# Optimization experiments

Measured on AMD Instinct MI355X. Metric: run time of the kernel, lower is better.

The kernel has to match this reference:

```python
import jax, jax.numpy as jnp
import numpy as np

FIELD_DIMS = [50000] * 24
NUM_FIELDS = len(FIELD_DIMS)
EMBED_DIM = 16
ATTN_SIZE = 32
TOTAL_VOCAB = int(np.sum(FIELD_DIMS))
OFFSETS = jnp.asarray(np.concatenate([[0], np.cumsum(FIELD_DIMS)[:-1]]), dtype=jnp.int64)
# all unordered field pairs (i < j)
_ROWS, _COLS = np.triu_indices(NUM_FIELDS, k=1)
ROWS = jnp.asarray(_ROWS)
COLS = jnp.asarray(_COLS)


def setup_inputs() -> dict:
    key = jax.random.key(0)
    ks = jax.random.split(key, 9)
    B = 16384
    x = jax.random.randint(ks[0], (B, NUM_FIELDS), 0, 50000, dtype=jnp.int64)
    s = 0.05
    return {
        "x": x,
        "embed_table": jax.random.normal(ks[1], (TOTAL_VOCAB, EMBED_DIM), jnp.float32) * s,
        "linear_table": jax.random.normal(ks[2], (TOTAL_VOCAB, 1), jnp.float32) * s,
        "linear_bias": jnp.zeros((1,), jnp.float32),
        "attn_W": jax.random.normal(ks[3], (EMBED_DIM, ATTN_SIZE), jnp.float32) * s,
        "attn_b": jnp.zeros((ATTN_SIZE,), jnp.float32),
        "proj_w": jax.random.normal(ks[4], (ATTN_SIZE, 1), jnp.float32) * s,
        "proj_b": jnp.zeros((1,), jnp.float32),
        "fc_w": jax.random.normal(ks[5], (EMBED_DIM, 1), jnp.float32) * s,
        "fc_b": jnp.zeros((1,), jnp.float32),
    }


def reference(x, embed_table, linear_table, linear_bias, attn_W, attn_b, proj_w, proj_b, fc_w, fc_b):
    idx = x + OFFSETS[None, :]                      # [B, F] global row ids
    emb = embed_table[idx]                          # [B, F, E]
    linear_term = linear_table[idx].sum(axis=1) + linear_bias  # [B, 1]
    # pairwise elementwise products
    inner = emb[:, ROWS, :] * emb[:, COLS, :]       # [B, P, E]
    # attention MLP over pairs
    h = jax.nn.relu(jnp.einsum('bpe,ea->bpa', inner, attn_W) + attn_b)  # [B, P, A]
    scores = jnp.einsum('bpa,ao->bpo', h, proj_w) + proj_b              # [B, P, 1]
    attn = jax.nn.softmax(scores, axis=1)           # softmax over pairs
    pooled = jnp.sum(attn * inner, axis=1)          # [B, E]
    cross_term = pooled @ fc_w + fc_b               # [B, 1]
    return linear_term + cross_term
```

## Files before the change

kernel.cpp:

```cpp
#include <hip/hip_runtime.h>
#include <hip/hip_bf16.h>
#include <float.h>


#define FN 24
#define ED 16
#define AS 32
#define NP 276
#define NT 9
#define LASTV 20
#define EPITCH 20
#define RPW 2
#define NTHR 256
#define FIELD_SIZE 50000

typedef __attribute__((ext_vector_type(8)))  short bf16x8;
typedef __attribute__((ext_vector_type(16))) float f32x16;
typedef __attribute__((ext_vector_type(2)))  float f32x2;

union BFR { int i[4]; bf16x8 v; };
union F4P { float4 f4; f32x2 p[2]; };

__device__ __forceinline__ short f2bf(float x) {
    union { __hip_bfloat16 h; short s; } u;
    u.h = __float2bfloat16(x);
    return u.s;
}

__device__ __forceinline__ void gather_embed(const float* __restrict__ et,
                                             int idxv, int lane,
                                             float4& a, float4& b) {
    const int f0 = lane >> 2, q0 = lane & 3;
    const int id0 = __shfl(idxv, f0, 64);
    const int id1 = __shfl(idxv, 16 + f0, 64);
    a = ((const float4*)(et + (size_t)id0 * ED))[q0];
    if (lane < 32)
        b = ((const float4*)(et + (size_t)id1 * ED))[q0];
}

__device__ __forceinline__ void write_embed(float* __restrict__ buf, int lane,
                                            const float4& a, const float4& b) {
    const int f0 = lane >> 2, q0 = lane & 3;
    *(float4*)&buf[f0 * EPITCH + q0 * 4] = a;
    if (lane < 32)
        *(float4*)&buf[(16 + f0) * EPITCH + q0 * 4] = b;
}

__global__ __launch_bounds__(NTHR, 4) void afm_kernel(
    const int*   __restrict__ x,
    const float* __restrict__ embed_table,
    const float* __restrict__ linear_table,
    const float* __restrict__ linear_bias,
    const float* __restrict__ attn_W,
    const float* __restrict__ attn_b,
    const float* __restrict__ proj_w,
    const float* __restrict__ fc_w,
    const float* __restrict__ fc_b,
    float*       __restrict__ out,
    int B)
{
    __shared__ float emb_s[NTHR / 64][2][FN * EPITCH];
    __shared__ int   pko_s[NT * 32];

    const int tid  = threadIdx.x;
    const int wave = tid >> 6;
    const int lane = tid & 63;
    const int half = lane >> 5;
    const int col  = lane & 31;
    const int e0   = half * 8;
    const int w0   = (blockIdx.x * (NTHR / 64) + wave) * RPW;

    for (int s = tid; s < NT * 32; s += NTHR) {
        const int p = (s < NP) ? s : (NP - 1);
        const int q = (NP - 1) - p;
        int m = (int)((sqrtf((float)(8 * q + 1)) + 1.0f) * 0.5f);
        if (m * (m + 1) / 2 <= q) ++m;
        if ((m - 1) * m / 2 > q) --m;
        const int fi = (FN - 1) - m;
        const int fj = fi + 1 + (p - (NP - m * (m + 1) / 2));
        pko_s[s] = ((fi * (EPITCH * 4)) << 16) | (fj * (EPITCH * 4));
    }

    int idxr[RPW];
#pragma unroll
    for (int k = 0; k < RPW; ++k) {
        const int r = w0 + k, rc = (r < B) ? r : (B - 1);
        idxr[k] = (lane < FN) ? (x[rc * FN + lane] + lane * FIELD_SIZE) : 0;
    }

    bf16x8 aW;
#pragma unroll
    for (int i = 0; i < 8; ++i) aW[i] = f2bf(attn_W[(e0 + i) * AS + col]);
    f32x16 biasC;
    f32x2  pw2[8];
#pragma unroll
    for (int r = 0; r < 16; ++r) {
        const int a = (r & 3) + 8 * (r >> 2) + 4 * half;
        biasC[r] = attn_b[a];
    }
#pragma unroll
    for (int r2 = 0; r2 < 8; ++r2) {
        const int a0 = (2 * r2 & 3) + 8 * (2 * r2 >> 2) + 4 * half;
        pw2[r2].x = proj_w[a0];
        pw2[r2].y = proj_w[a0 + 1];
    }
    f32x2 fcw2[4];
#pragma unroll
    for (int i = 0; i < 4; ++i) {
        fcw2[i].x = fc_w[e0 + 2 * i];
        fcw2[i].y = fc_w[e0 + 2 * i + 1];
    }
    const float cbias = linear_bias[0] + fc_b[0];

    float linv = (lane < FN) ? linear_table[idxr[0]] : 0.f;
    {
        float4 ga, gb;
        gather_embed(embed_table, idxr[0], lane, ga, gb);
        write_embed(emb_s[wave][0], lane, ga, gb);
    }

    __syncthreads();
    int pk[NT];
#pragma unroll
    for (int t = 0; t < NT; ++t) pk[t] = pko_s[t * 32 + col];

#pragma unroll
    for (int k = 0; k < RPW; ++k) {
        const int row = w0 + k;
        float4 na, nb; float linn = 0.f;
        if (k + 1 < RPW) {
            linn = (lane < FN) ? linear_table[idxr[k + 1]] : 0.f;
            gather_embed(embed_table, idxr[k + 1], lane, na, nb);
        }

        const char* embb = (const char*)emb_s[wave][k & 1] + half * 32;
        float m = -FLT_MAX, ssum = 0.f, gacc = 0.f;
#pragma unroll
        for (int t = 0; t < NT; ++t) {
            const int oi = pk[t] >> 16;
            const int oj = pk[t] & 0xffff;
            F4P xi0, xi1, xj0, xj1;
            xi0.f4 = *(const float4*)(embb + oi);
            xi1.f4 = *(const float4*)(embb + oi + 16);
            xj0.f4 = *(const float4*)(embb + oj);
            xj1.f4 = *(const float4*)(embb + oj + 16);
            const f32x2 P0 = xi0.p[0] * xj0.p[0];
            const f32x2 P1 = xi0.p[1] * xj0.p[1];
            const f32x2 P2 = xi1.p[0] * xj1.p[0];
            const f32x2 P3 = xi1.p[1] * xj1.p[1];
            f32x2 G = P0 * fcw2[0];
            G = __builtin_elementwise_fma(P1, fcw2[1], G);
            G = __builtin_elementwise_fma(P2, fcw2[2], G);
            G = __builtin_elementwise_fma(P3, fcw2[3], G);
            const float gv = G.x + G.y;
            BFR u;
            u.i[0] = __builtin_amdgcn_perm(__float_as_int(P0.y), __float_as_int(P0.x), 0x07060302);
            u.i[1] = __builtin_amdgcn_perm(__float_as_int(P1.y), __float_as_int(P1.x), 0x07060302);
            u.i[2] = __builtin_amdgcn_perm(__float_as_int(P2.y), __float_as_int(P2.x), 0x07060302);
            u.i[3] = __builtin_amdgcn_perm(__float_as_int(P3.y), __float_as_int(P3.x), 0x07060302);
            const f32x16 c = __builtin_amdgcn_mfma_f32_32x32x16_bf16(aW, u.v, biasC, 0, 0, 0);
            f32x2 sac; sac.x = 0.f; sac.y = 0.f;
            f32x2 z2;  z2.x = 0.f;  z2.y = 0.f;
#pragma unroll
            for (int r2 = 0; r2 < 8; ++r2) {
                f32x2 h; h.x = c[2 * r2]; h.y = c[2 * r2 + 1];
                h = __builtin_elementwise_max(h, z2);
                sac = __builtin_elementwise_fma(h, pw2[r2], sac);
            }
            float s = sac.x + sac.y;
            s += __shfl_xor(s, 32, 64);
            const bool valid = (t < NT - 1) || (col < LASTV);
            s = valid ? s : -FLT_MAX;
            const float mn   = fmaxf(m, s);
            const float cold = __expf(m - mn);
            const float e    = __expf(s - mn);
            ssum = fmaf(ssum, cold, e);
            gacc = fmaf(gacc, cold, e * gv);
            m = mn;
        }

        float M = m;
#pragma unroll
        for (int off = 16; off; off >>= 1) M = fmaxf(M, __shfl_xor(M, off, 64));
        const float rs = __expf(m - M);
        ssum *= rs; gacc *= rs;
#pragma unroll
        for (int off = 16; off; off >>= 1) ssum += __shfl_xor(ssum, off, 64);
#pragma unroll
        for (int off = 32; off; off >>= 1) gacc += __shfl_xor(gacc, off, 64);
        float lin = linv;
#pragma unroll
        for (int off = 32; off; off >>= 1) lin += __shfl_xor(lin, off, 64);

        if (row < B && lane == 0)
            out[row] = lin + cbias + gacc / ssum;

        if (k + 1 < RPW) {
            write_embed(emb_s[wave][(k + 1) & 1], lane, na, nb);
            linv = linn;
        }
    }
}

extern "C" void kernel_launch(void* const* d_in, const int* in_sizes, int n_in,
                              void* d_out, int out_size, void* d_ws, size_t ws_size,
                              hipStream_t stream) {
    const int*   x            = (const int*)  d_in[0];
    const float* embed_table  = (const float*)d_in[1];
    const float* linear_table = (const float*)d_in[2];
    const float* linear_bias  = (const float*)d_in[3];
    const float* attn_W       = (const float*)d_in[4];
    const float* attn_b       = (const float*)d_in[5];
    const float* proj_w       = (const float*)d_in[6];
    const float* fc_w         = (const float*)d_in[8];
    const float* fc_b         = (const float*)d_in[9];
    float* out = (float*)d_out;

    const int B = in_sizes[0] / FN;
    const int rows_per_block = (NTHR / 64) * RPW;
    const int grid = (B + rows_per_block - 1) / rows_per_block;
    afm_kernel<<<grid, NTHR, 0, stream>>>(x, embed_table, linear_table,
                                          linear_bias, attn_W, attn_b, proj_w,
                                          fc_w, fc_b, out, B);
}
```

Before: 142.8 us.

## Process one row per wave and replace online softmax with two-pass softmax

Each wave now handles a single batch row instead of two, which removes the double-buffered prefetch of the next row's embeddings and doubles the grid size. Scores and fc-projected values for all pair tiles are kept in registers, and the softmax is done in two passes (global max, then exp-sum) instead of the online rescaling recurrence. The intent is fewer expf calls, a shorter dependency chain and more parallel waves to hide gather latency. The cost is losing the software pipelining of the next row's gather and repeating per-block setup (pair table, weights) for every row.

```diff
diff --git a/kernel.cpp b/kernel.cpp
--- a/kernel.cpp
+++ b/kernel.cpp
@@ -10,7 +10,6 @@
 #define NT 9
 #define LASTV 20
 #define EPITCH 20
-#define RPW 2
 #define NTHR 256
 #define FIELD_SIZE 50000
 
@@ -27,25 +26,6 @@
     return u.s;
 }
 
-__device__ __forceinline__ void gather_embed(const float* __restrict__ et,
-                                             int idxv, int lane,
-                                             float4& a, float4& b) {
-    const int f0 = lane >> 2, q0 = lane & 3;
-    const int id0 = __shfl(idxv, f0, 64);
-    const int id1 = __shfl(idxv, 16 + f0, 64);
-    a = ((const float4*)(et + (size_t)id0 * ED))[q0];
-    if (lane < 32)
-        b = ((const float4*)(et + (size_t)id1 * ED))[q0];
-}
-
-__device__ __forceinline__ void write_embed(float* __restrict__ buf, int lane,
-                                            const float4& a, const float4& b) {
-    const int f0 = lane >> 2, q0 = lane & 3;
-    *(float4*)&buf[f0 * EPITCH + q0 * 4] = a;
-    if (lane < 32)
-        *(float4*)&buf[(16 + f0) * EPITCH + q0 * 4] = b;
-}
-
 __global__ __launch_bounds__(NTHR, 4) void afm_kernel(
     const int*   __restrict__ x,
     const float* __restrict__ embed_table,
@@ -59,7 +39,7 @@
     float*       __restrict__ out,
     int B)
 {
-    __shared__ float emb_s[NTHR / 64][2][FN * EPITCH];
+    __shared__ float emb_s[NTHR / 64][FN * EPITCH];
     __shared__ int   pko_s[NT * 32];
 
     const int tid  = threadIdx.x;
@@ -68,7 +48,8 @@
     const int half = lane >> 5;
     const int col  = lane & 31;
     const int e0   = half * 8;
-    const int w0   = (blockIdx.x * (NTHR / 64) + wave) * RPW;
+    const int row  = blockIdx.x * (NTHR / 64) + wave;
+    const int rowc = (row < B) ? row : (B - 1);
 
     for (int s = tid; s < NT * 32; s += NTHR) {
         const int p = (s < NP) ? s : (NP - 1);
@@ -81,11 +62,20 @@
         pko_s[s] = ((fi * (EPITCH * 4)) << 16) | (fj * (EPITCH * 4));
     }
 
-    int idxr[RPW];
-#pragma unroll
-    for (int k = 0; k < RPW; ++k) {
-        const int r = w0 + k, rc = (r < B) ? r : (B - 1);
-        idxr[k] = (lane < FN) ? (x[rc * FN + lane] + lane * FIELD_SIZE) : 0;
+    const int idxv = (lane < FN) ? (x[rowc * FN + lane] + lane * FIELD_SIZE) : 0;
+    const float linv = (lane < FN) ? linear_table[idxv] : 0.f;
+
+    {
+        float* emb = emb_s[wave];
+        const int f0 = lane >> 2, q0 = lane & 3;
+        const int id0 = __shfl(idxv, f0, 64);
+        const int id1 = __shfl(idxv, 16 + f0, 64);
+        const float4 a = ((const float4*)(embed_table + (size_t)id0 * ED))[q0];
+        *(float4*)&emb[f0 * EPITCH + q0 * 4] = a;
+        if (lane < 32) {
+            const float4 b = ((const float4*)(embed_table + (size_t)id1 * ED))[q0];
+            *(float4*)&emb[(16 + f0) * EPITCH + q0 * 4] = b;
+        }
     }
 
     bf16x8 aW;
@@ -112,94 +102,71 @@
     }
     const float cbias = linear_bias[0] + fc_b[0];
 
-    float linv = (lane < FN) ? linear_table[idxr[0]] : 0.f;
-    {
-        float4 ga, gb;
-        gather_embed(embed_table, idxr[0], lane, ga, gb);
-        write_embed(emb_s[wave][0], lane, ga, gb);
+    __syncthreads();
+
+    const char* embb = (const char*)emb_s[wave] + half * 32;
+    float sc[NT], g[NT];
+#pragma unroll
+    for (int t = 0; t < NT; ++t) {
+        const int pkv = pko_s[t * 32 + col];
+        const int oi = pkv >> 16;
+        const int oj = pkv & 0xffff;
+        F4P xi0, xi1, xj0, xj1;
+        xi0.f4 = *(const float4*)(embb + oi);
+        xi1.f4 = *(const float4*)(embb + oi + 16);
+        xj0.f4 = *(const float4*)(embb + oj);
+        xj1.f4 = *(const float4*)(embb + oj + 16);
+        const f32x2 P0 = xi0.p[0] * xj0.p[0];
+        const f32x2 P1 = xi0.p[1] * xj0.p[1];
+        const f32x2 P2 = xi1.p[0] * xj1.p[0];
+        const f32x2 P3 = xi1.p[1] * xj1.p[1];
+        f32x2 G = P0 * fcw2[0];
+        G = __builtin_elementwise_fma(P1, fcw2[1], G);
+        G = __builtin_elementwise_fma(P2, fcw2[2], G);
+        G = __builtin_elementwise_fma(P3, fcw2[3], G);
+        g[t] = G.x + G.y;
+        BFR u;
+        u.i[0] = __builtin_amdgcn_perm(__float_as_int(P0.y), __float_as_int(P0.x), 0x07060302);
+        u.i[1] = __builtin_amdgcn_perm(__float_as_int(P1.y), __float_as_int(P1.x), 0x07060302);
+        u.i[2] = __builtin_amdgcn_perm(__float_as_int(P2.y), __float_as_int(P2.x), 0x07060302);
+        u.i[3] = __builtin_amdgcn_perm(__float_as_int(P3.y), __float_as_int(P3.x), 0x07060302);
+        const f32x16 c = __builtin_amdgcn_mfma_f32_32x32x16_bf16(aW, u.v, biasC, 0, 0, 0);
+        f32x2 sac; sac.x = 0.f; sac.y = 0.f;
+        f32x2 z2;  z2.x = 0.f;  z2.y = 0.f;
+#pragma unroll
+        for (int r2 = 0; r2 < 8; ++r2) {
+            f32x2 h; h.x = c[2 * r2]; h.y = c[2 * r2 + 1];
+            h = __builtin_elementwise_max(h, z2);
+            sac = __builtin_elementwise_fma(h, pw2[r2], sac);
+        }
+        sc[t] = sac.x + sac.y;
     }
 
-    __syncthreads();
-    int pk[NT];
 #pragma unroll
-    for (int t = 0; t < NT; ++t) pk[t] = pko_s[t * 32 + col];
+    for (int t = 0; t < NT; ++t) sc[t] += __shfl_xor(sc[t], 32, 64);
+    float M = sc[0];
+#pragma unroll
+    for (int t = 1; t < NT; ++t) M = fmaxf(M, sc[t]);
+#pragma unroll
+    for (int off = 16; off; off >>= 1) M = fmaxf(M, __shfl_xor(M, off, 64));
+    float ssum = 0.f, cp = 0.f;
+#pragma unroll
+    for (int t = 0; t < NT; ++t) {
+        float e = __expf(sc[t] - M);
+        if (t == NT - 1) e = (col < LASTV) ? e : 0.f;
+        ssum += e;
+        cp = fmaf(e, g[t], cp);
+    }
+#pragma unroll
+    for (int off = 16; off; off >>= 1) ssum += __shfl_xor(ssum, off, 64);
+#pragma unroll
+    for (int off = 32; off; off >>= 1) cp += __shfl_xor(cp, off, 64);
+    float lin = linv;
+#pragma unroll
+    for (int off = 32; off; off >>= 1) lin += __shfl_xor(lin, off, 64);
 
-#pragma unroll
-    for (int k = 0; k < RPW; ++k) {
-        const int row = w0 + k;
-        float4 na, nb; float linn = 0.f;
-        if (k + 1 < RPW) {
-            linn = (lane < FN) ? linear_table[idxr[k + 1]] : 0.f;
-            gather_embed(embed_table, idxr[k + 1], lane, na, nb);
-        }
-
-        const char* embb = (const char*)emb_s[wave][k & 1] + half * 32;
-        float m = -FLT_MAX, ssum = 0.f, gacc = 0.f;
-#pragma unroll
-        for (int t = 0; t < NT; ++t) {
-            const int oi = pk[t] >> 16;
-            const int oj = pk[t] & 0xffff;
-            F4P xi0, xi1, xj0, xj1;
-            xi0.f4 = *(const float4*)(embb + oi);
-            xi1.f4 = *(const float4*)(embb + oi + 16);
-            xj0.f4 = *(const float4*)(embb + oj);
-            xj1.f4 = *(const float4*)(embb + oj + 16);
-            const f32x2 P0 = xi0.p[0] * xj0.p[0];
-            const f32x2 P1 = xi0.p[1] * xj0.p[1];
-            const f32x2 P2 = xi1.p[0] * xj1.p[0];
-            const f32x2 P3 = xi1.p[1] * xj1.p[1];
-            f32x2 G = P0 * fcw2[0];
-            G = __builtin_elementwise_fma(P1, fcw2[1], G);
-            G = __builtin_elementwise_fma(P2, fcw2[2], G);
-            G = __builtin_elementwise_fma(P3, fcw2[3], G);
-            const float gv = G.x + G.y;
-            BFR u;
-            u.i[0] = __builtin_amdgcn_perm(__float_as_int(P0.y), __float_as_int(P0.x), 0x07060302);
-            u.i[1] = __builtin_amdgcn_perm(__float_as_int(P1.y), __float_as_int(P1.x), 0x07060302);
-            u.i[2] = __builtin_amdgcn_perm(__float_as_int(P2.y), __float_as_int(P2.x), 0x07060302);
-            u.i[3] = __builtin_amdgcn_perm(__float_as_int(P3.y), __float_as_int(P3.x), 0x07060302);
-            const f32x16 c = __builtin_amdgcn_mfma_f32_32x32x16_bf16(aW, u.v, biasC, 0, 0, 0);
-            f32x2 sac; sac.x = 0.f; sac.y = 0.f;
-            f32x2 z2;  z2.x = 0.f;  z2.y = 0.f;
-#pragma unroll
-            for (int r2 = 0; r2 < 8; ++r2) {
-                f32x2 h; h.x = c[2 * r2]; h.y = c[2 * r2 + 1];
-                h = __builtin_elementwise_max(h, z2);
-                sac = __builtin_elementwise_fma(h, pw2[r2], sac);
-            }
-            float s = sac.x + sac.y;
-            s += __shfl_xor(s, 32, 64);
-            const bool valid = (t < NT - 1) || (col < LASTV);
-            s = valid ? s : -FLT_MAX;
-            const float mn   = fmaxf(m, s);
-            const float cold = __expf(m - mn);
-            const float e    = __expf(s - mn);
-            ssum = fmaf(ssum, cold, e);
-            gacc = fmaf(gacc, cold, e * gv);
-            m = mn;
-        }
-
-        float M = m;
-#pragma unroll
-        for (int off = 16; off; off >>= 1) M = fmaxf(M, __shfl_xor(M, off, 64));
-        const float rs = __expf(m - M);
-        ssum *= rs; gacc *= rs;
-#pragma unroll
-        for (int off = 16; off; off >>= 1) ssum += __shfl_xor(ssum, off, 64);
-#pragma unroll
-        for (int off = 32; off; off >>= 1) gacc += __shfl_xor(gacc, off, 64);
-        float lin = linv;
-#pragma unroll
-        for (int off = 32; off; off >>= 1) lin += __shfl_xor(lin, off, 64);
-
-        if (row < B && lane == 0)
-            out[row] = lin + cbias + gacc / ssum;
-
-        if (k + 1 < RPW) {
-            write_embed(emb_s[wave][(k + 1) & 1], lane, na, nb);
-            linv = linn;
-        }
-    }
+    if (row < B && lane == 0)
+        out[row] = lin + cbias + cp / ssum;
 }
 
 extern "C" void kernel_launch(void* const* d_in, const int* in_sizes, int n_in,
@@ -217,7 +184,7 @@
     float* out = (float*)d_out;
 
     const int B = in_sizes[0] / FN;
-    const int rows_per_block = (NTHR / 64) * RPW;
+    const int rows_per_block = NTHR / 64;
     const int grid = (B + rows_per_block - 1) / rows_per_block;
     afm_kernel<<<grid, NTHR, 0, stream>>>(x, embed_table, linear_table,
                                           linear_bias, attn_W, attn_b, proj_w,
```

Result: no change. 145.4 us (+1.8%).
